# Kernel tuning notes

Measured on AMD Instinct MI355X. Metric: run time of the kernel, lower is better.

Reference implementation:

```python
import jax, jax.numpy as jnp
import numpy as np

E, DIN, H, DOUT, B = 16, 128, 512, 64, 8192


def _init_linear(key, e, fan_in, fan_out):
    # mimic torch nn.Linear default init: U(-1/sqrt(fan_in), 1/sqrt(fan_in))
    kw, kb = jax.random.split(key)
    bound = 1.0 / np.sqrt(fan_in)
    W = jax.random.uniform(kw, (e, fan_in, fan_out), jnp.float32, -bound, bound)
    b = jax.random.uniform(kb, (e, fan_out), jnp.float32, -bound, bound)
    return W, b


def setup_inputs() -> dict:
    key = jax.random.key(0)
    kx, k1, k2, k3 = jax.random.split(key, 4)
    x = jax.random.normal(kx, (B, E, DIN), jnp.float32)
    W1, b1 = _init_linear(k1, E, DIN, H)
    W2, b2 = _init_linear(k2, E, H, H)
    W3, b3 = _init_linear(k3, E, H, DOUT)
    return {"x": x, "W1": W1, "b1": b1, "W2": W2, "b2": b2, "W3": W3, "b3": b3}


def reference(x, W1, b1, W2, b2, W3, b3):
    # per-expert 3-layer MLP, batched over the expert dim as grouped GEMMs
    h = jax.nn.relu(jnp.einsum('bei,eih->beh', x, W1) + b1)        # [B,E,H]
    h = jax.nn.relu(jnp.einsum('beh,ehg->beg', h, W2) + b2)        # [B,E,H]
    o = jnp.einsum('beh,eho->beo', h, W3) + b3                     # [B,E,DOUT]
    return jnp.sum(o, axis=1)                                      # [B,DOUT]
```

## Files before the change

kernel.cpp:

```cpp
#include <hip/hip_runtime.h>


#define NE   16
#define NDIN 128
#define NH   512
#define NDO  64
#define NB   8192
#define EG   4

using bf16x8 = __attribute__((ext_vector_type(8))) __bf16;
using bf16x4 = __attribute__((ext_vector_type(4))) __bf16;
using f32x4  = __attribute__((ext_vector_type(4))) float;

__device__ __forceinline__ unsigned short f2bf(float f) {
    union { float f; unsigned u; } v; v.f = f;
    unsigned r = v.u + 0x7FFFu + ((v.u >> 16) & 1u);
    return (unsigned short)(r >> 16);
}

__device__ __forceinline__ bf16x8 cvt8(float4 a, float4 b) {
    bf16x8 r;
    r[0] = (__bf16)a.x; r[1] = (__bf16)a.y; r[2] = (__bf16)a.z; r[3] = (__bf16)a.w;
    r[4] = (__bf16)b.x; r[5] = (__bf16)b.y; r[6] = (__bf16)b.z; r[7] = (__bf16)b.w;
    return r;
}

__device__ __forceinline__ int shidx(int m, int n) {
    return m * NH + (((n >> 3) ^ (m & 15)) << 3) + (n & 7);
}
__device__ __forceinline__ int shx(int m, int n) {
    return m * NDIN + ((((n >> 3) ^ (m & 15)) & 15) << 3) + (n & 7);
}

__global__ __launch_bounds__(256) void prep_weights(
    const float* __restrict__ W1, const float* __restrict__ W2, const float* __restrict__ W3,
    unsigned short* __restrict__ W1f, unsigned short* __restrict__ W2f, unsigned short* __restrict__ W3f,
    float* __restrict__ out)
{
    __shared__ float lds[32][521];
    const int job = blockIdx.x, tt = threadIdx.x;
    if (job < 64) {
        float4* oz = (float4*)(out + (size_t)job * 8192);
        const float4 z = {0.f, 0.f, 0.f, 0.f};
#pragma unroll
        for (int i = 0; i < 8; ++i) oz[i * 256 + tt] = z;
    }
    const float* src; unsigned short* dst; int e, kt, C, NKT, isW3;
    if (job < 64)       { e = job >> 2;                kt = job & 3;  src = W1; dst = W1f; C = NH;  NKT = 4;  isW3 = 0; }
    else if (job < 320) { int q = job - 64;  e = q >> 4; kt = q & 15; src = W2; dst = W2f; C = NH;  NKT = 16; isW3 = 0; }
    else                { int q = job - 320; e = q >> 4; kt = q & 15; src = W3; dst = W3f; C = NDO; NKT = 16; isW3 = 1; }

    const float* s = src + ((size_t)e * (NKT * 32) + kt * 32) * C;
    const int nf4 = (32 * C) >> 2;
    for (int i = tt; i < nf4; i += 256) {
        const int r = i / (C >> 2), c4 = (i % (C >> 2)) * 4;
        const float4 v = *(const float4*)(s + (size_t)r * C + c4);
        lds[r][c4 + 0] = v.x; lds[r][c4 + 1] = v.y;
        lds[r][c4 + 2] = v.z; lds[r][c4 + 3] = v.w;
    }
    __syncthreads();

    const int npair = (C >> 4) * 64;
    for (int p = tt; p < npair; p += 256) {
        const int t = p >> 6, lane = p & 63, q = lane >> 4, l16 = lane & 15;
        union { unsigned short u[8]; uint4 v; } pk;
#pragma unroll
        for (int j = 0; j < 8; ++j) pk.u[j] = f2bf(lds[q * 8 + j][t * 16 + l16]);
        size_t off;
        if (isW3) off = (((size_t)e * 4 + t) * 16 + kt) * 512 + lane * 8;
        else      off = ((((size_t)e * 8 + (t >> 2)) * NKT + kt) * 4 + (t & 3)) * 512 + lane * 8;
        *(uint4*)(dst + off) = pk.v;
    }
}

__global__ __launch_bounds__(512, 2) void moe_fused(
    const float* __restrict__ x,
    const float* __restrict__ b1,
    const float* __restrict__ b2,
    const float* __restrict__ b3,
    const unsigned short* __restrict__ W1f,
    const unsigned short* __restrict__ W2f,
    const unsigned short* __restrict__ W3f,
    float* __restrict__ out)
{
    __shared__ unsigned short sMem[64 * NDIN + 2 * 64 * NH];
    unsigned short* sX  = sMem;
    unsigned short* sHA = sMem + 64 * NDIN;
    unsigned short* sHB = sHA + 64 * NH;

    const int tid  = threadIdx.x;
    const int wave = tid >> 6;
    const int lane = tid & 63;
    const int q    = lane >> 4;
    const int l16  = lane & 15;
    const int hi2  = l16 >> 2;
    const int lo2  = l16 & 3;
    const int qe   = (q ^ lo2) * 8;

    const int lin = blockIdx.x;
    const int xcd = lin & 7;
    const int eg  = xcd >> 1;
    const int rt  = ((lin >> 3) << 1) | (xcd & 1);
    const int b0  = rt << 6;

    int aH[4], aX[4];
#pragma unroll
    for (int m = 0; m < 4; ++m) {
        aH[m] = (m * 16 + l16) * NH   + qe;
        aX[m] = (m * 16 + l16) * NDIN + qe;
    }
    const int r0 = tid >> 4, c8 = (tid & 15) * 8;

    const int n3 = wave & 3, mp = wave >> 2;
    int a3[2];
#pragma unroll
    for (int i = 0; i < 2; ++i) a3[i] = ((2 * mp + i) * 16 + l16) * NH + qe;

    bf16x8 bfr[3][4], afr[3][4];

    f32x4 oacc[2];
    oacc[0] = {0.f, 0.f, 0.f, 0.f}; oacc[1] = {0.f, 0.f, 0.f, 0.f};
    float bacc = 0.f;

    {
        const int e0 = eg * EG;
        const float* p0 = x + ((size_t)(b0 + r0)      * NE + e0) * NDIN + c8;
        const float* p1 = x + ((size_t)(b0 + 32 + r0) * NE + e0) * NDIN + c8;
        float4 u0 = *(const float4*)p0, u1 = *(const float4*)(p0 + 4);
        float4 u2 = *(const float4*)p1, u3 = *(const float4*)(p1 + 4);
        *(bf16x8*)&sX[shx(r0, c8)]      = cvt8(u0, u1);
        *(bf16x8*)&sX[shx(32 + r0, c8)] = cvt8(u2, u3);
    }
    __syncthreads();

#pragma unroll 1
    for (int ei = 0; ei < EG; ++ei) {
        const int e = eg * EG + ei;

        const unsigned short* b1p = W1f + (size_t)e * NH * NDIN + wave * 8192  + lane * 8;
        const unsigned short* b2p = W2f + (size_t)e * NH * NH   + wave * 32768 + lane * 8;

#pragma unroll
        for (int s = 0; s < 2; ++s)
#pragma unroll
            for (int n = 0; n < 4; ++n)
                bfr[s][n] = *(const bf16x8*)(b1p + s * 2048 + n * 512);
        float4 b1q[4];
#pragma unroll
        for (int n = 0; n < 4; ++n)
            b1q[n] = *(const float4*)(b1 + e * NH + wave * 64 + n * 16 + q * 4);

        f32x4 acc[4][4];
#pragma unroll
        for (int n = 0; n < 4; ++n) {
            const f32x4 bi = {b1q[n].x, b1q[n].y, b1q[n].z, b1q[n].w};
#pragma unroll
            for (int m = 0; m < 4; ++m) acc[m][n] = bi;
        }
#pragma unroll
        for (int s = 0; s < 2; ++s)
#pragma unroll
            for (int m = 0; m < 4; ++m)
                afr[s][m] = *(const bf16x8*)&sX[aX[m] + (((s ^ hi2) & 3) << 5)];

#pragma unroll
        for (int kt = 0; kt < 4; ++kt) {
            const int cur = kt % 3, pre = (kt + 2) % 3;
            if (kt < 2) {
#pragma unroll
                for (int n = 0; n < 4; ++n)
                    bfr[pre][n] = *(const bf16x8*)(b1p + (kt + 2) * 2048 + n * 512);
#pragma unroll
                for (int m = 0; m < 4; ++m)
                    afr[pre][m] = *(const bf16x8*)&sX[aX[m] + ((((kt + 2) ^ hi2) & 3) << 5)];
            }
#pragma unroll
            for (int m = 0; m < 4; ++m)
#pragma unroll
                for (int n = 0; n < 4; ++n)
                    acc[m][n] = __builtin_amdgcn_mfma_f32_16x16x32_bf16(
                        bfr[cur][n], afr[cur][m], acc[m][n], 0, 0, 0);
        }

#pragma unroll
        for (int s = 0; s < 2; ++s)
#pragma unroll
            for (int n = 0; n < 4; ++n)
                bfr[s][n] = *(const bf16x8*)(b2p + s * 2048 + n * 512);
        float4 b2q[4];
#pragma unroll
        for (int n = 0; n < 4; ++n)
            b2q[n] = *(const float4*)(b2 + e * NH + wave * 64 + n * 16 + q * 4);

#pragma unroll
        for (int n = 0; n < 4; ++n) {
            const int c0 = wave * 64 + n * 16 + q * 4;
#pragma unroll
            for (int m = 0; m < 4; ++m) {
                bf16x4 pk;
#pragma unroll
                for (int r = 0; r < 4; ++r) pk[r] = (__bf16)fmaxf(acc[m][n][r], 0.f);
                *(bf16x4*)&sHA[shidx(m * 16 + l16, c0)] = pk;
            }
        }
        __syncthreads();

        f32x4 acc2[4][4];
#pragma unroll
        for (int n = 0; n < 4; ++n) {
            const f32x4 bi = {b2q[n].x, b2q[n].y, b2q[n].z, b2q[n].w};
#pragma unroll
            for (int m = 0; m < 4; ++m) acc2[m][n] = bi;
        }
#pragma unroll
        for (int s = 0; s < 2; ++s)
#pragma unroll
            for (int m = 0; m < 4; ++m)
                afr[s][m] = *(const bf16x8*)&sHA[aH[m] + (((s ^ hi2)) << 5)];

#pragma unroll
        for (int kt = 0; kt < 16; ++kt) {
            const int cur = kt % 3, pre = (kt + 2) % 3;
            if (kt < 14) {
#pragma unroll
                for (int n = 0; n < 4; ++n)
                    bfr[pre][n] = *(const bf16x8*)(b2p + (kt + 2) * 2048 + n * 512);
#pragma unroll
                for (int m = 0; m < 4; ++m)
                    afr[pre][m] = *(const bf16x8*)&sHA[aH[m] + ((((kt + 2) ^ hi2)) << 5)];
            }
#pragma unroll
            for (int m = 0; m < 4; ++m)
#pragma unroll
                for (int n = 0; n < 4; ++n)
                    acc2[m][n] = __builtin_amdgcn_mfma_f32_16x16x32_bf16(
                        bfr[cur][n], afr[cur][m], acc2[m][n], 0, 0, 0);
        }

        const unsigned short* b3p = W3f + (size_t)e * NDO * NH + n3 * 8192 + lane * 8;
        bf16x8 b3f[8];
#pragma unroll
        for (int j = 0; j < 8; ++j) b3f[j] = *(const bf16x8*)(b3p + j * 512);
        const float b3v = b3[e * NDO + n3 * 16 + l16];

        float4 xu0, xu1, xu2, xu3;
        {
            const int en = eg * EG + ((ei + 1) & (EG - 1));
            const float* pn0 = x + ((size_t)(b0 + r0)      * NE + en) * NDIN + c8;
            const float* pn1 = x + ((size_t)(b0 + 32 + r0) * NE + en) * NDIN + c8;
            xu0 = *(const float4*)pn0; xu1 = *(const float4*)(pn0 + 4);
            xu2 = *(const float4*)pn1; xu3 = *(const float4*)(pn1 + 4);
        }

#pragma unroll
        for (int n = 0; n < 4; ++n) {
            const int c0 = wave * 64 + n * 16 + q * 4;
#pragma unroll
            for (int m = 0; m < 4; ++m) {
                bf16x4 pk;
#pragma unroll
                for (int r = 0; r < 4; ++r) pk[r] = (__bf16)fmaxf(acc2[m][n][r], 0.f);
                *(bf16x4*)&sHB[shidx(m * 16 + l16, c0)] = pk;
            }
        }
        *(bf16x8*)&sX[shx(r0, c8)]      = cvt8(xu0, xu1);
        *(bf16x8*)&sX[shx(32 + r0, c8)] = cvt8(xu2, xu3);
        __syncthreads();

        bf16x8 a3f[4][2];
#pragma unroll
        for (int s = 0; s < 3; ++s)
#pragma unroll
            for (int i = 0; i < 2; ++i)
                a3f[s][i] = *(const bf16x8*)&sHB[a3[i] + (((s ^ hi2)) << 5)];

#pragma unroll
        for (int kt = 0; kt < 16; ++kt) {
            const int cur = kt & 3;
            if (kt < 13) {
                const int pre = (kt + 3) & 3;
#pragma unroll
                for (int i = 0; i < 2; ++i)
                    a3f[pre][i] = *(const bf16x8*)&sHB[a3[i] + ((((kt + 3) ^ hi2)) << 5)];
            }
#pragma unroll
            for (int i = 0; i < 2; ++i)
                oacc[i] = __builtin_amdgcn_mfma_f32_16x16x32_bf16(
                    a3f[cur][i], b3f[kt & 7], oacc[i], 0, 0, 0);
            if (kt < 8)
                b3f[kt & 7] = *(const bf16x8*)(b3p + (kt + 8) * 512);
        }
        bacc += b3v;
    }

#pragma unroll
    for (int i = 0; i < 2; ++i) {
        const int col = n3 * 16 + l16;
#pragma unroll
        for (int r = 0; r < 4; ++r) {
            const int row = b0 + (2 * mp + i) * 16 + q * 4 + r;
            unsafeAtomicAdd(out + (size_t)row * NDO + col, oacc[i][r] + bacc);
        }
    }
}

extern "C" void kernel_launch(void* const* d_in, const int* in_sizes, int n_in,
                              void* d_out, int out_size, void* d_ws, size_t ws_size,
                              hipStream_t stream) {
    const float* x  = (const float*)d_in[0];
    const float* W1 = (const float*)d_in[1];
    const float* b1 = (const float*)d_in[2];
    const float* W2 = (const float*)d_in[3];
    const float* b2 = (const float*)d_in[4];
    const float* W3 = (const float*)d_in[5];
    const float* b3 = (const float*)d_in[6];
    float* out = (float*)d_out;

    unsigned short* W1f = (unsigned short*)d_ws;
    unsigned short* W2f = W1f + (size_t)NE * NH * NDIN;
    unsigned short* W3f = W2f + (size_t)NE * NH * NH;

    prep_weights<<<dim3(576), 256, 0, stream>>>(W1, W2, W3, W1f, W2f, W3f, out);
    moe_fused<<<dim3((NB / 64) * (NE / EG)), 512, 0, stream>>>(x, b1, b2, b3, W1f, W2f, W3f, out);
}
```

Measured before the change: 205.0 us.

## Deepen weight prefetch pipeline and prefetch next expert's W1 across layers

Raises the W2 register prefetch from a 3-slot to a 4-slot ring, so weight tiles are loaded three k-steps ahead. The first W1 tiles and b1 for the next expert are now loaded during the layer-3 phase of the current expert, hiding the global-load latency at the start of each expert. To fit the extra live registers, launch bounds drop from 2 to 1 blocks per CU, which reduces occupancy and may cut latency hiding from other wavefronts.

```diff
diff --git a/kernel.cpp b/kernel.cpp
--- a/kernel.cpp
+++ b/kernel.cpp
@@ -73,7 +73,7 @@
     }
 }
 
-__global__ __launch_bounds__(512, 2) void moe_fused(
+__global__ __launch_bounds__(512, 1) void moe_fused(
     const float* __restrict__ x,
     const float* __restrict__ b1,
     const float* __restrict__ b2,
@@ -116,7 +116,8 @@
 #pragma unroll
     for (int i = 0; i < 2; ++i) a3[i] = ((2 * mp + i) * 16 + l16) * NH + qe;
 
-    bf16x8 bfr[3][4], afr[3][4];
+    bf16x8 bfr[4][4], afr[3][4];
+    float4 b1q[4];
 
     f32x4 oacc[2];
     oacc[0] = {0.f, 0.f, 0.f, 0.f}; oacc[1] = {0.f, 0.f, 0.f, 0.f};
@@ -130,6 +131,15 @@
         float4 u2 = *(const float4*)p1, u3 = *(const float4*)(p1 + 4);
         *(bf16x8*)&sX[shx(r0, c8)]      = cvt8(u0, u1);
         *(bf16x8*)&sX[shx(32 + r0, c8)] = cvt8(u2, u3);
+        const unsigned short* b1p0 = W1f + (size_t)e0 * NH * NDIN + wave * 8192 + lane * 8;
+#pragma unroll
+        for (int s = 0; s < 2; ++s)
+#pragma unroll
+            for (int n = 0; n < 4; ++n)
+                bfr[s][n] = *(const bf16x8*)(b1p0 + s * 2048 + n * 512);
+#pragma unroll
+        for (int n = 0; n < 4; ++n)
+            b1q[n] = *(const float4*)(b1 + e0 * NH + wave * 64 + n * 16 + q * 4);
     }
     __syncthreads();
 
@@ -140,16 +150,6 @@
         const unsigned short* b1p = W1f + (size_t)e * NH * NDIN + wave * 8192  + lane * 8;
         const unsigned short* b2p = W2f + (size_t)e * NH * NH   + wave * 32768 + lane * 8;
 
-#pragma unroll
-        for (int s = 0; s < 2; ++s)
-#pragma unroll
-            for (int n = 0; n < 4; ++n)
-                bfr[s][n] = *(const bf16x8*)(b1p + s * 2048 + n * 512);
-        float4 b1q[4];
-#pragma unroll
-        for (int n = 0; n < 4; ++n)
-            b1q[n] = *(const float4*)(b1 + e * NH + wave * 64 + n * 16 + q * 4);
-
         f32x4 acc[4][4];
 #pragma unroll
         for (int n = 0; n < 4; ++n) {
@@ -165,25 +165,24 @@
 
 #pragma unroll
         for (int kt = 0; kt < 4; ++kt) {
-            const int cur = kt % 3, pre = (kt + 2) % 3;
             if (kt < 2) {
 #pragma unroll
                 for (int n = 0; n < 4; ++n)
-                    bfr[pre][n] = *(const bf16x8*)(b1p + (kt + 2) * 2048 + n * 512);
+                    bfr[(kt + 2) & 3][n] = *(const bf16x8*)(b1p + (kt + 2) * 2048 + n * 512);
 #pragma unroll
                 for (int m = 0; m < 4; ++m)
-                    afr[pre][m] = *(const bf16x8*)&sX[aX[m] + ((((kt + 2) ^ hi2) & 3) << 5)];
+                    afr[(kt + 2) % 3][m] = *(const bf16x8*)&sX[aX[m] + ((((kt + 2) ^ hi2) & 3) << 5)];
             }
 #pragma unroll
             for (int m = 0; m < 4; ++m)
 #pragma unroll
                 for (int n = 0; n < 4; ++n)
                     acc[m][n] = __builtin_amdgcn_mfma_f32_16x16x32_bf16(
-                        bfr[cur][n], afr[cur][m], acc[m][n], 0, 0, 0);
-        }
-
-#pragma unroll
-        for (int s = 0; s < 2; ++s)
+                        bfr[kt & 3][n], afr[kt % 3][m], acc[m][n], 0, 0, 0);
+        }
+
+#pragma unroll
+        for (int s = 0; s < 3; ++s)
 #pragma unroll
             for (int n = 0; n < 4; ++n)
                 bfr[s][n] = *(const bf16x8*)(b2p + s * 2048 + n * 512);
@@ -220,36 +219,46 @@
 
 #pragma unroll
         for (int kt = 0; kt < 16; ++kt) {
-            const int cur = kt % 3, pre = (kt + 2) % 3;
-            if (kt < 14) {
-#pragma unroll
-                for (int n = 0; n < 4; ++n)
-                    bfr[pre][n] = *(const bf16x8*)(b2p + (kt + 2) * 2048 + n * 512);
+            if (kt < 13)
+#pragma unroll
+                for (int n = 0; n < 4; ++n)
+                    bfr[(kt + 3) & 3][n] = *(const bf16x8*)(b2p + (kt + 3) * 2048 + n * 512);
+            if (kt < 14)
 #pragma unroll
                 for (int m = 0; m < 4; ++m)
-                    afr[pre][m] = *(const bf16x8*)&sHA[aH[m] + ((((kt + 2) ^ hi2)) << 5)];
-            }
+                    afr[(kt + 2) % 3][m] = *(const bf16x8*)&sHA[aH[m] + ((((kt + 2) ^ hi2)) << 5)];
 #pragma unroll
             for (int m = 0; m < 4; ++m)
 #pragma unroll
                 for (int n = 0; n < 4; ++n)
                     acc2[m][n] = __builtin_amdgcn_mfma_f32_16x16x32_bf16(
-                        bfr[cur][n], afr[cur][m], acc2[m][n], 0, 0, 0);
-        }
-
-        const unsigned short* b3p = W3f + (size_t)e * NDO * NH + n3 * 8192 + lane * 8;
+                        bfr[kt & 3][n], afr[kt % 3][m], acc2[m][n], 0, 0, 0);
+        }
+
+        const unsigned short* b3p = W3f + ((size_t)e * 4 + n3) * 8192 + lane * 8;
         bf16x8 b3f[8];
 #pragma unroll
         for (int j = 0; j < 8; ++j) b3f[j] = *(const bf16x8*)(b3p + j * 512);
         const float b3v = b3[e * NDO + n3 * 16 + l16];
 
+        const int en = eg * EG + ((ei + 1) & (EG - 1));
         float4 xu0, xu1, xu2, xu3;
         {
-            const int en = eg * EG + ((ei + 1) & (EG - 1));
             const float* pn0 = x + ((size_t)(b0 + r0)      * NE + en) * NDIN + c8;
             const float* pn1 = x + ((size_t)(b0 + 32 + r0) * NE + en) * NDIN + c8;
             xu0 = *(const float4*)pn0; xu1 = *(const float4*)(pn0 + 4);
             xu2 = *(const float4*)pn1; xu3 = *(const float4*)(pn1 + 4);
+        }
+        {
+            const unsigned short* b1pn = W1f + (size_t)en * NH * NDIN + wave * 8192 + lane * 8;
+#pragma unroll
+            for (int s = 0; s < 2; ++s)
+#pragma unroll
+                for (int n = 0; n < 4; ++n)
+                    bfr[s][n] = *(const bf16x8*)(b1pn + s * 2048 + n * 512);
+#pragma unroll
+            for (int n = 0; n < 4; ++n)
+                b1q[n] = *(const float4*)(b1 + en * NH + wave * 64 + n * 16 + q * 4);
         }
 
 #pragma unroll
```

Result: slower. 212.1 us (+3.5%).
